# Kernel tuning notes

Measured on AMD Instinct MI355X. Metric: run time of the kernel, lower is better.

Reference implementation:

```python
import jax, jax.numpy as jnp
import numpy as np

THRESH = 0.9
NUM_HEADS = 4
HEAD_DIM = 8


def _ln(x, g, b, eps=1e-5):
    m = x.mean(-1, keepdims=True)
    v = ((x - m) ** 2).mean(-1, keepdims=True)
    return (x - m) * jax.lax.rsqrt(v + eps) * g + b


def setup_inputs() -> dict:
    key = jax.random.key(0)
    ks = jax.random.split(key, 32)
    n, d_in, h1, h2, d, ffn, nb = 4096, 512, 128, 64, 32, 64, 2

    def w(k, shape, fan_in):
        return jax.random.normal(k, shape, jnp.float32) * (1.0 / np.sqrt(fan_in))

    inp = {}
    inp["x"] = jax.random.normal(ks[0], (n, d_in), jnp.float32)
    # Autoencoder encoder: input_dim -> 128 -> 64 -> latent_dim
    inp["enc_w1"] = w(ks[1], (d_in, h1), d_in); inp["enc_b1"] = jnp.zeros((h1,), jnp.float32)
    inp["enc_w2"] = w(ks[2], (h1, h2), h1);     inp["enc_b2"] = jnp.zeros((h2,), jnp.float32)
    inp["enc_w3"] = w(ks[3], (h2, d), h2);      inp["enc_b3"] = jnp.zeros((d,), jnp.float32)
    # Transformer blocks (stacked over num_blocks=2)
    inp["wq"] = w(ks[4], (nb, d, d), d); inp["bq"] = jnp.zeros((nb, d), jnp.float32)
    inp["wk"] = w(ks[5], (nb, d, d), d); inp["bk"] = jnp.zeros((nb, d), jnp.float32)
    inp["wv"] = w(ks[6], (nb, d, d), d); inp["bv"] = jnp.zeros((nb, d), jnp.float32)
    inp["wo"] = w(ks[7], (nb, d, d), d); inp["bo"] = jnp.zeros((nb, d), jnp.float32)
    inp["ln1_g"] = jnp.ones((nb, d), jnp.float32);  inp["ln1_b"] = jnp.zeros((nb, d), jnp.float32)
    inp["ffn_w1"] = w(ks[8], (nb, d, ffn), d);      inp["ffn_b1"] = jnp.zeros((nb, ffn), jnp.float32)
    inp["ffn_w2"] = w(ks[9], (nb, ffn, d), ffn);    inp["ffn_b2"] = jnp.zeros((nb, d), jnp.float32)
    inp["ln2_g"] = jnp.ones((nb, d), jnp.float32);  inp["ln2_b"] = jnp.zeros((nb, d), jnp.float32)
    # Head: Linear(d,16) -> Tanh -> Linear(16, num_classes)
    inp["head_w1"] = w(ks[10], (d, 16), d);  inp["head_b1"] = jnp.zeros((16,), jnp.float32)
    inp["head_w2"] = w(ks[11], (16, 1), 16); inp["head_b2"] = jnp.zeros((1,), jnp.float32)
    return inp


def reference(x, enc_w1, enc_b1, enc_w2, enc_b2, enc_w3, enc_b3,
              wq, bq, wk, bk, wv, bv, wo, bo,
              ln1_g, ln1_b, ffn_w1, ffn_b1, ffn_w2, ffn_b2, ln2_g, ln2_b,
              head_w1, head_b1, head_w2, head_b2):
    # --- autoencoder encode: [n, d_in] -> [n, d] ---
    a = jax.nn.relu(x @ enc_w1 + enc_b1)
    a = jax.nn.relu(a @ enc_w2 + enc_b2)
    latent = a @ enc_w3 + enc_b3  # [n, d]

    # --- graph pool: cosine-sim threshold mask, per-node masked neighbor mean ---
    # self-similarity is 1.0 >= THRESH, so every node has >=1 neighbor (deg>=1)
    norms = jnp.linalg.norm(latent, axis=1, keepdims=True) + 1e-12
    normed = latent / norms
    sims = normed @ normed.T                                  # [n, n]
    mask = (sims >= THRESH).astype(latent.dtype)              # [n, n]
    deg = mask.sum(axis=1, keepdims=True)                     # [n, 1]
    pooled = latent + (mask @ latent) / deg                   # latent[i] + mean of neighbors

    # --- transformer blocks (post-LN, eval mode: dropout off) ---
    h = pooled[None]  # [1, n, d]
    n, d = pooled.shape
    nb = wq.shape[0]
    scale = 1.0 / np.sqrt(HEAD_DIM)
    for i in range(nb):
        q = (h @ wq[i] + bq[i]).reshape(1, n, NUM_HEADS, HEAD_DIM)
        k = (h @ wk[i] + bk[i]).reshape(1, n, NUM_HEADS, HEAD_DIM)
        v = (h @ wv[i] + bv[i]).reshape(1, n, NUM_HEADS, HEAD_DIM)
        scores = jnp.einsum('bqhd,bkhd->bhqk', q, k) * scale  # [1, H, n, n]
        attn = jax.nn.softmax(scores, axis=-1)
        o = jnp.einsum('bhqk,bkhd->bqhd', attn, v).reshape(1, n, d)
        o = o @ wo[i] + bo[i]
        h = _ln(h + o, ln1_g[i], ln1_b[i])
        f = jax.nn.relu(h @ ffn_w1[i] + ffn_b1[i]) @ ffn_w2[i] + ffn_b2[i]
        h = _ln(h + f, ln2_g[i], ln2_b[i])

    # --- head on mean-pooled sequence ---
    m = h.mean(axis=1)  # [1, d]
    out = jnp.tanh(m @ head_w1 + head_b1) @ head_w2 + head_b2  # [1, 1]
    return out.squeeze()
```

## Files before the change

kernel.cpp:

```cpp
#include <hip/hip_runtime.h>
#include <math.h>

#define N 4096
#define DIN 512
#define D 32
#define JC 8

__global__ __launch_bounds__(256) void enc_kernel(
    const float* __restrict__ x,
    const float* __restrict__ w1, const float* __restrict__ b1,
    const float* __restrict__ w2, const float* __restrict__ b2,
    const float* __restrict__ w3, const float* __restrict__ b3,
    float* __restrict__ latent, float* __restrict__ normed) {
  __shared__ float xs[8][512];
  __shared__ float h1p[4][8][128];
  __shared__ float h1s[8][128];
  __shared__ float h2s[8][64];
  __shared__ float w2s[128][64];
  __shared__ float w3s[64][32];
  const int t = threadIdx.x;
  const int r0 = blockIdx.x * 8;

  const float4* xg = (const float4*)(x + (size_t)r0 * DIN);
  float4* xl = (float4*)&xs[0][0];
#pragma unroll
  for (int i = 0; i < 4; ++i) xl[t + i * 256] = xg[t + i * 256];
  float4* w2l = (float4*)&w2s[0][0];
  const float4* w2g = (const float4*)w2;
#pragma unroll
  for (int i = 0; i < 8; ++i) w2l[t + i * 256] = w2g[t + i * 256];
  float4* w3l = (float4*)&w3s[0][0];
  const float4* w3g = (const float4*)w3;
#pragma unroll
  for (int i = 0; i < 2; ++i) w3l[t + i * 256] = w3g[t + i * 256];
  __syncthreads();

  {
    const int jc2 = (t & 63) * 2;
    const int kq = t >> 6;
    const int kb = kq * 128;
    float a0[8], a1[8];
#pragma unroll
    for (int r = 0; r < 8; ++r) { a0[r] = 0.f; a1[r] = 0.f; }
    const float* wp = w1 + (size_t)kb * 128 + jc2;

#define ENC_LD4(P0, P1, P2, P3, KK)                          \
    P0 = *(const float2*)&wp[(size_t)(KK) * 128];            \
    P1 = *(const float2*)&wp[(size_t)((KK) + 1) * 128];      \
    P2 = *(const float2*)&wp[(size_t)((KK) + 2) * 128];      \
    P3 = *(const float2*)&wp[(size_t)((KK) + 3) * 128];

#define ENC_STEP(W0, WA, WB, WC, KK)                                   \
    {                                                                  \
      _Pragma("unroll")                                                \
      for (int r = 0; r < 8; ++r) {                                    \
        const float4 xv = *(const float4*)&xs[r][kb + (KK)];           \
        a0[r] = fmaf(xv.x, W0.x, a0[r]); a1[r] = fmaf(xv.x, W0.y, a1[r]); \
        a0[r] = fmaf(xv.y, WA.x, a0[r]); a1[r] = fmaf(xv.y, WA.y, a1[r]); \
        a0[r] = fmaf(xv.z, WB.x, a0[r]); a1[r] = fmaf(xv.z, WB.y, a1[r]); \
        a0[r] = fmaf(xv.w, WC.x, a0[r]); a1[r] = fmaf(xv.w, WC.y, a1[r]); \
      }                                                                \
    }

    float2 A0, A1, A2, A3, B0, B1, B2, B3, C0, C1, C2, C3, D0, D1, D2, D3;
    ENC_LD4(A0, A1, A2, A3, 0)
    ENC_LD4(B0, B1, B2, B3, 4)
    ENC_LD4(C0, C1, C2, C3, 8)
    ENC_LD4(D0, D1, D2, D3, 12)
    for (int kk = 0; kk < 128; kk += 16) {
      ENC_STEP(A0, A1, A2, A3, kk + 0);
      if (kk + 16 < 128) { ENC_LD4(A0, A1, A2, A3, kk + 16) }
      ENC_STEP(B0, B1, B2, B3, kk + 4);
      if (kk + 20 < 128) { ENC_LD4(B0, B1, B2, B3, kk + 20) }
      ENC_STEP(C0, C1, C2, C3, kk + 8);
      if (kk + 24 < 128) { ENC_LD4(C0, C1, C2, C3, kk + 24) }
      ENC_STEP(D0, D1, D2, D3, kk + 12);
      if (kk + 28 < 128) { ENC_LD4(D0, D1, D2, D3, kk + 28) }
    }
#undef ENC_STEP
#undef ENC_LD4
#pragma unroll
    for (int r = 0; r < 8; ++r) {
      h1p[kq][r][jc2] = a0[r];
      h1p[kq][r][jc2 + 1] = a1[r];
    }
  }
  __syncthreads();

#pragma unroll
  for (int e0 = 0; e0 < 1024; e0 += 256) {
    const int e = e0 + t;
    const int r = e >> 7, c = e & 127;
    const float s = b1[c] + ((h1p[0][r][c] + h1p[1][r][c]) + (h1p[2][r][c] + h1p[3][r][c]));
    h1s[r][c] = fmaxf(s, 0.f);
  }
  __syncthreads();

  {
    const int j = t & 63, rg = t >> 6;
    const int ra = rg * 2, rb = ra + 1;
    float a0 = b2[j], a1 = b2[j];
#pragma unroll 8
    for (int kk = 0; kk < 128; ++kk) {
      const float w = w2s[kk][j];
      a0 = fmaf(h1s[ra][kk], w, a0);
      a1 = fmaf(h1s[rb][kk], w, a1);
    }
    h2s[ra][j] = fmaxf(a0, 0.f);
    h2s[rb][j] = fmaxf(a1, 0.f);
  }
  __syncthreads();

  {
    const int j = t & 31, og = t >> 5;
    float acc = b3[j];
#pragma unroll 8
    for (int kk = 0; kk < 64; ++kk) acc = fmaf(h2s[og][kk], w3s[kk][j], acc);
    float s2 = acc * acc;
    s2 += __shfl_xor(s2, 1);
    s2 += __shfl_xor(s2, 2);
    s2 += __shfl_xor(s2, 4);
    s2 += __shfl_xor(s2, 8);
    s2 += __shfl_xor(s2, 16);
    const float inv = 1.0f / (sqrtf(s2) + 1e-12f);
    const size_t off = (size_t)(r0 + og) * D + j;
    latent[off] = acc;
    normed[off] = acc * inv;
  }
}

__global__ __launch_bounds__(256) void pool_kernel(const float* __restrict__ normed,
                                                   const float* __restrict__ latent,
                                                   float* __restrict__ pacc,
                                                   float* __restrict__ pdeg) {
  __shared__ float smem[8192 + 256];
  float* nt = smem;
  float* lt = smem + 4096;
  float* degr = smem + 8192;
  const int t = threadIdx.x;
  const int il = t & 63, g = t >> 6;
  const int i0 = blockIdx.x * 64;
  const int j0 = blockIdx.y * 512;

  float ni[32];
  const float* nrow = normed + (size_t)(i0 + il) * D;
#pragma unroll
  for (int c = 0; c < 32; ++c) ni[c] = nrow[c];

  float acc[32];
#pragma unroll
  for (int c = 0; c < 32; ++c) acc[c] = 0.f;
  float deg = 0.f;

  for (int jt = j0; jt < j0 + 512; jt += 128) {
    __syncthreads();
    const float4* ng = (const float4*)(normed + (size_t)jt * D);
    const float4* lg = (const float4*)(latent + (size_t)jt * D);
    float4* ntl = (float4*)nt;
    float4* ltl = (float4*)lt;
#pragma unroll
    for (int i = 0; i < 4; ++i) {
      ntl[t + i * 256] = ng[t + i * 256];
      ltl[t + i * 256] = lg[t + i * 256];
    }
    __syncthreads();
    for (int jj = g; jj < 128; jj += 4) {
      const float* nr = nt + jj * 32;
      float s = 0.f;
#pragma unroll
      for (int c = 0; c < 32; ++c) s = fmaf(ni[c], nr[c], s);
      if (s >= 0.9f) {
        deg += 1.f;
        const float* lrow = lt + jj * 32;
#pragma unroll
        for (int c = 0; c < 32; ++c) acc[c] += lrow[c];
      }
    }
  }
  __syncthreads();
  float* accr = smem;
#pragma unroll
  for (int c = 0; c < 32; ++c) accr[(g * 64 + il) * 32 + c] = acc[c];
  degr[t] = deg;
  __syncthreads();
  for (int e = t; e < 64 * 32; e += 256) {
    const float s = accr[e] + accr[2048 + e] + accr[4096 + e] + accr[6144 + e];
    pacc[((size_t)blockIdx.y * N + i0 + (e >> 5)) * 32 + (e & 31)] = s;
  }
  if (t < 64) {
    pdeg[(size_t)blockIdx.y * N + i0 + t] = degr[t] + degr[64 + t] + degr[128 + t] + degr[192 + t];
  }
}

__global__ __launch_bounds__(256) void pool_combine(const float* __restrict__ latent,
                                                    const float* __restrict__ pacc,
                                                    const float* __restrict__ pdeg,
                                                    float* __restrict__ h) {
  const int e = blockIdx.x * 256 + threadIdx.x;
  const int i = e >> 5;
  float s = 0.f, dg = 0.f;
#pragma unroll
  for (int gch = 0; gch < JC; ++gch) {
    s += pacc[(size_t)gch * N * 32 + e];
    dg += pdeg[(size_t)gch * N + i];
  }
  h[e] = latent[e] + s / dg;
}

__global__ __launch_bounds__(256) void qkv_kernel(
    const float* __restrict__ h,
    const float* __restrict__ wq, const float* __restrict__ bq,
    const float* __restrict__ wk, const float* __restrict__ bk,
    const float* __restrict__ wv, const float* __restrict__ bv,
    float* __restrict__ q, float* __restrict__ k, float* __restrict__ v,
    int* __restrict__ kmax2i) {
  __shared__ float hs[32][32];
  __shared__ float wsm[3][32][32];
  __shared__ int kred[4];
  const int t = threadIdx.x;
  const int r0 = blockIdx.x * 32;
  if (t < 4) kred[t] = 0;
  ((float4*)&hs[0][0])[t] = ((const float4*)(h + (size_t)r0 * 32))[t];
  ((float4*)&wsm[0][0][0])[t] = ((const float4*)wq)[t];
  ((float4*)&wsm[1][0][0])[t] = ((const float4*)wk)[t];
  ((float4*)&wsm[2][0][0])[t] = ((const float4*)wv)[t];
  __syncthreads();
  const int j = t & 31, og = t >> 5;
  const int head = j >> 3;
  float aq[4], ak[4], av[4];
#pragma unroll
  for (int u = 0; u < 4; ++u) { aq[u] = bq[j]; ak[u] = bk[j]; av[u] = bv[j]; }
  for (int kk = 0; kk < 32; ++kk) {
    const float wqv = wsm[0][kk][j], wkv = wsm[1][kk][j], wvv = wsm[2][kk][j];
#pragma unroll
    for (int u = 0; u < 4; ++u) {
      const float hh = hs[og * 4 + u][kk];
      aq[u] = fmaf(hh, wqv, aq[u]);
      ak[u] = fmaf(hh, wkv, ak[u]);
      av[u] = fmaf(hh, wvv, av[u]);
    }
  }
  const float scale = 1.4426950408889634f * 0.35355339059327373f;
#pragma unroll
  for (int u = 0; u < 4; ++u) {
    const size_t off = (size_t)(r0 + og * 4 + u) * 32 + j;
    q[off] = aq[u] * scale;
    k[off] = ak[u];
    v[off] = av[u];
  }
#pragma unroll
  for (int u = 0; u < 4; ++u) {
    float s2 = ak[u] * ak[u];
    s2 += __shfl_xor(s2, 1);
    s2 += __shfl_xor(s2, 2);
    s2 += __shfl_xor(s2, 4);
    if ((j & 7) == 0) atomicMax(&kred[head], __float_as_int(s2));
  }
  __syncthreads();
  if (t < 4) atomicMax(&kmax2i[t], kred[t]);
}

__global__ __launch_bounds__(256) __attribute__((amdgpu_waves_per_eu(2, 2)))
void attn_kernel(const float* __restrict__ q,
                 const float* __restrict__ k,
                 const float* __restrict__ v,
                 const int* __restrict__ kmax2i,
                 float* __restrict__ apacc,
                 float* __restrict__ apl) {
  __shared__ float4 tiles[1024];
  float4* kls = tiles;
  float4* vls = tiles + 512;
  const int t = threadIdx.x;
  const int jg = t & 7, head = (t >> 3) & 3, rg = t >> 5;
  const int r0 = blockIdx.x * 64;
  const int j0 = blockIdx.y * (N / JC);

  const float km2 = __int_as_float(kmax2i[head]);

  float4 qa[8], qb[8], accA[8], accB[8];
  float mneg[8], l[8];
#pragma unroll
  for (int u = 0; u < 8; ++u) {
    const float* qr = q + (size_t)(r0 + rg * 8 + u) * 32 + head * 8;
    qa[u] = ((const float4*)qr)[0];
    qb[u] = ((const float4*)qr)[1];
    const float qn2 = qa[u].x * qa[u].x + qa[u].y * qa[u].y + qa[u].z * qa[u].z + qa[u].w * qa[u].w +
                      qb[u].x * qb[u].x + qb[u].y * qb[u].y + qb[u].z * qb[u].z + qb[u].w * qb[u].w;
    mneg[u] = -sqrtf(qn2 * km2);
    l[u] = 0.f;
    accA[u] = make_float4(0.f, 0.f, 0.f, 0.f);
    accB[u] = make_float4(0.f, 0.f, 0.f, 0.f);
  }

  float4 kr0, kr1, vr0, vr1;
  {
    const float4* kg = (const float4*)(k + (size_t)j0 * 32);
    const float4* vg = (const float4*)(v + (size_t)j0 * 32);
    kr0 = kg[t]; kr1 = kg[t + 256];
    vr0 = vg[t]; vr1 = vg[t + 256];
  }

  const int rA = t >> 3, slotA = (t & 7) ^ (rA & 7);
  const int g1 = t + 256;
  const int rB = g1 >> 3, slotB = (g1 & 7) ^ (rB & 7);

  const int h2 = head * 2;
  const int s0 = h2 ^ jg, s1 = (h2 + 1) ^ jg;
  for (int jt = j0; jt < j0 + (N / JC); jt += 64) {
    __syncthreads();
    kls[rA * 8 + slotA] = kr0;
    kls[rB * 8 + slotB] = kr1;
    vls[rA * 8 + slotA] = vr0;
    vls[rB * 8 + slotB] = vr1;
    __syncthreads();
    if (jt + 64 < j0 + (N / JC)) {
      const float4* kg = (const float4*)(k + (size_t)(jt + 64) * 32);
      const float4* vg = (const float4*)(v + (size_t)(jt + 64) * 32);
      kr0 = kg[t]; kr1 = kg[t + 256];
      vr0 = vg[t]; vr1 = vg[t + 256];
    }
#pragma unroll 2
    for (int it = 0; it < 8; ++it) {
      const int jj = it * 8 + jg;
      const float4 ka = kls[jj * 8 + s0];
      const float4 kb = kls[jj * 8 + s1];
      const float4 va = vls[jj * 8 + s0];
      const float4 vb = vls[jj * 8 + s1];
#pragma unroll
      for (int u = 0; u < 8; ++u) {
        float s = fmaf(qa[u].x, ka.x, mneg[u]);
        s = fmaf(qa[u].y, ka.y, s);
        s = fmaf(qa[u].z, ka.z, s);
        s = fmaf(qa[u].w, ka.w, s);
        s = fmaf(qb[u].x, kb.x, s);
        s = fmaf(qb[u].y, kb.y, s);
        s = fmaf(qb[u].z, kb.z, s);
        s = fmaf(qb[u].w, kb.w, s);
        const float p = __builtin_amdgcn_exp2f(s);
        l[u] += p;
        accA[u].x = fmaf(p, va.x, accA[u].x);
        accA[u].y = fmaf(p, va.y, accA[u].y);
        accA[u].z = fmaf(p, va.z, accA[u].z);
        accA[u].w = fmaf(p, va.w, accA[u].w);
        accB[u].x = fmaf(p, vb.x, accB[u].x);
        accB[u].y = fmaf(p, vb.y, accB[u].y);
        accB[u].z = fmaf(p, vb.z, accB[u].z);
        accB[u].w = fmaf(p, vb.w, accB[u].w);
      }
    }
  }
#pragma unroll
  for (int u = 0; u < 8; ++u) {
#pragma unroll
    for (int m = 1; m <= 4; m <<= 1) {
      accA[u].x += __shfl_xor(accA[u].x, m);
      accA[u].y += __shfl_xor(accA[u].y, m);
      accA[u].z += __shfl_xor(accA[u].z, m);
      accA[u].w += __shfl_xor(accA[u].w, m);
      accB[u].x += __shfl_xor(accB[u].x, m);
      accB[u].y += __shfl_xor(accB[u].y, m);
      accB[u].z += __shfl_xor(accB[u].z, m);
      accB[u].w += __shfl_xor(accB[u].w, m);
      l[u] += __shfl_xor(l[u], m);
    }
  }
  if (jg == 0) {
#pragma unroll
    for (int u = 0; u < 8; ++u) {
      const int row = r0 + rg * 8 + u;
      float* ap = apacc + (size_t)blockIdx.y * N * 32 + (size_t)row * 32 + head * 8;
      ((float4*)ap)[0] = accA[u];
      ((float4*)ap)[1] = accB[u];
      apl[(size_t)blockIdx.y * N * 4 + (size_t)row * 4 + head] = l[u];
    }
  }
}

__global__ __launch_bounds__(256) void acombine(const float* __restrict__ apacc,
                                                const float* __restrict__ apl,
                                                float* __restrict__ attno) {
  const int e = blockIdx.x * 256 + threadIdx.x;
  const int row = e >> 5;
  const int hh = (e >> 3) & 3;
  float L = 0.f, S = 0.f;
#pragma unroll
  for (int jc = 0; jc < JC; ++jc) {
    L += apl[(size_t)jc * N * 4 + row * 4 + hh];
    S += apacc[(size_t)jc * N * 32 + e];
  }
  attno[e] = S / L;
}

__global__ __launch_bounds__(256) void oln1_kernel(const float* __restrict__ attno,
                                                   const float* __restrict__ wo,
                                                   const float* __restrict__ bo,
                                                   const float* __restrict__ g,
                                                   const float* __restrict__ b,
                                                   float* __restrict__ h) {
  __shared__ float als[32][32];
  __shared__ float wols[32][32];
  __shared__ float ys[32][33];
  const int t = threadIdx.x;
  const int r0 = blockIdx.x * 32;
  ((float4*)&als[0][0])[t] = ((const float4*)(attno + (size_t)r0 * 32))[t];
  ((float4*)&wols[0][0])[t] = ((const float4*)wo)[t];
  __syncthreads();
  const int j = t & 31, og = t >> 5;
  float acc[4];
#pragma unroll
  for (int u = 0; u < 4; ++u) acc[u] = bo[j];
  for (int kk = 0; kk < 32; ++kk) {
    const float w = wols[kk][j];
#pragma unroll
    for (int u = 0; u < 4; ++u) acc[u] = fmaf(als[og * 4 + u][kk], w, acc[u]);
  }
#pragma unroll
  for (int u = 0; u < 4; ++u) {
    const int r = og * 4 + u;
    ys[r][j] = h[(size_t)(r0 + r) * 32 + j] + acc[u];
  }
  __syncthreads();
  if (t < 32) {
    float mu = 0.f;
#pragma unroll
    for (int c = 0; c < 32; ++c) mu += ys[t][c];
    mu *= (1.f / 32.f);
    float var = 0.f;
#pragma unroll
    for (int c = 0; c < 32; ++c) {
      const float dd = ys[t][c] - mu;
      var = fmaf(dd, dd, var);
    }
    var *= (1.f / 32.f);
    const float rs = rsqrtf(var + 1e-5f);
#pragma unroll
    for (int c = 0; c < 32; ++c)
      h[(size_t)(r0 + t) * 32 + c] = (ys[t][c] - mu) * rs * g[c] + b[c];
  }
}

__global__ __launch_bounds__(256) void ffn_kernel(const float* __restrict__ hin,
                                                  const float* __restrict__ w1,
                                                  const float* __restrict__ b1,
                                                  const float* __restrict__ w2,
                                                  const float* __restrict__ b2,
                                                  const float* __restrict__ g,
                                                  const float* __restrict__ bb,
                                                  float* __restrict__ h) {
  __shared__ float hs[32][32];
  __shared__ float w1s[32][64];
  __shared__ float w2s[64][32];
  __shared__ float mids[32][64];
  __shared__ float ys[32][33];
  const int t = threadIdx.x;
  const int r0 = blockIdx.x * 32;
  ((float4*)&hs[0][0])[t] = ((const float4*)(hin + (size_t)r0 * 32))[t];
#pragma unroll
  for (int i = 0; i < 2; ++i) {
    ((float4*)&w1s[0][0])[t + i * 256] = ((const float4*)w1)[t + i * 256];
    ((float4*)&w2s[0][0])[t + i * 256] = ((const float4*)w2)[t + i * 256];
  }
  __syncthreads();
  {
    const int jm = t & 63, gg = t >> 6;
    float acc[8];
#pragma unroll
    for (int u = 0; u < 8; ++u) acc[u] = b1[jm];
    for (int kk = 0; kk < 32; ++kk) {
      const float w = w1s[kk][jm];
#pragma unroll
      for (int u = 0; u < 8; ++u) acc[u] = fmaf(hs[gg * 8 + u][kk], w, acc[u]);
    }
#pragma unroll
    for (int u = 0; u < 8; ++u) mids[gg * 8 + u][jm] = fmaxf(acc[u], 0.f);
  }
  __syncthreads();
  {
    const int j = t & 31, og = t >> 5;
    float acc[4];
#pragma unroll
    for (int u = 0; u < 4; ++u) acc[u] = b2[j];
    for (int kk = 0; kk < 64; ++kk) {
      const float w = w2s[kk][j];
#pragma unroll
      for (int u = 0; u < 4; ++u) acc[u] = fmaf(mids[og * 4 + u][kk], w, acc[u]);
    }
#pragma unroll
    for (int u = 0; u < 4; ++u) {
      const int r = og * 4 + u;
      ys[r][j] = hs[r][j] + acc[u];
    }
  }
  __syncthreads();
  if (t < 32) {
    float mu = 0.f;
#pragma unroll
    for (int c = 0; c < 32; ++c) mu += ys[t][c];
    mu *= (1.f / 32.f);
    float var = 0.f;
#pragma unroll
    for (int c = 0; c < 32; ++c) {
      const float dd = ys[t][c] - mu;
      var = fmaf(dd, dd, var);
    }
    var *= (1.f / 32.f);
    const float rs = rsqrtf(var + 1e-5f);
#pragma unroll
    for (int c = 0; c < 32; ++c)
      h[(size_t)(r0 + t) * 32 + c] = (ys[t][c] - mu) * rs * g[c] + bb[c];
  }
}

__global__ __launch_bounds__(256) void headp_kernel(const float* __restrict__ h,
                                                    float* __restrict__ partial) {
  __shared__ float red[8][32];
  const int t = threadIdx.x;
  const int c = t & 31, rg = t >> 5;
  const int r0 = blockIdx.x * 64;
  float s = 0.f;
#pragma unroll
  for (int u = 0; u < 8; ++u) s += h[(size_t)(r0 + rg * 8 + u) * 32 + c];
  red[rg][c] = s;
  __syncthreads();
  if (t < 32) {
    float ss = 0.f;
#pragma unroll
    for (int u = 0; u < 8; ++u) ss += red[u][t];
    partial[blockIdx.x * 32 + t] = ss;
  }
}

__global__ __launch_bounds__(64) void headf_kernel(const float* __restrict__ partial,
                                                   const float* __restrict__ w1,
                                                   const float* __restrict__ b1,
                                                   const float* __restrict__ w2,
                                                   const float* __restrict__ b2,
                                                   float* __restrict__ out) {
  __shared__ float mls[32];
  __shared__ float tls[16];
  const int t = threadIdx.x;
  if (t < 32) {
    float s = 0.f;
    for (int bb = 0; bb < 64; ++bb) s += partial[bb * 32 + t];
    mls[t] = s * (1.f / 4096.f);
  }
  __syncthreads();
  if (t < 16) {
    float a = b1[t];
#pragma unroll
    for (int c = 0; c < 32; ++c) a = fmaf(mls[c], w1[c * 16 + t], a);
    tls[t] = tanhf(a);
  }
  __syncthreads();
  if (t == 0) {
    float o = b2[0];
#pragma unroll
    for (int jj = 0; jj < 16; ++jj) o = fmaf(tls[jj], w2[jj], o);
    out[0] = o;
  }
}

extern "C" void kernel_launch(void* const* d_in, const int* in_sizes, int n_in,
                              void* d_out, int out_size, void* d_ws, size_t ws_size,
                              hipStream_t stream) {
  const float* x      = (const float*)d_in[0];
  const float* enc_w1 = (const float*)d_in[1];
  const float* enc_b1 = (const float*)d_in[2];
  const float* enc_w2 = (const float*)d_in[3];
  const float* enc_b2 = (const float*)d_in[4];
  const float* enc_w3 = (const float*)d_in[5];
  const float* enc_b3 = (const float*)d_in[6];
  const float* wq     = (const float*)d_in[7];
  const float* bq     = (const float*)d_in[8];
  const float* wk     = (const float*)d_in[9];
  const float* bk     = (const float*)d_in[10];
  const float* wv     = (const float*)d_in[11];
  const float* bv     = (const float*)d_in[12];
  const float* wo     = (const float*)d_in[13];
  const float* bo     = (const float*)d_in[14];
  const float* ln1_g  = (const float*)d_in[15];
  const float* ln1_b  = (const float*)d_in[16];
  const float* ffn_w1 = (const float*)d_in[17];
  const float* ffn_b1 = (const float*)d_in[18];
  const float* ffn_w2 = (const float*)d_in[19];
  const float* ffn_b2 = (const float*)d_in[20];
  const float* ln2_g  = (const float*)d_in[21];
  const float* ln2_b  = (const float*)d_in[22];
  const float* head_w1 = (const float*)d_in[23];
  const float* head_b1 = (const float*)d_in[24];
  const float* head_w2 = (const float*)d_in[25];
  const float* head_b2 = (const float*)d_in[26];

  float* ws      = (float*)d_ws;
  float* latent  = ws;
  float* normed  = ws + 131072;
  float* h       = ws + 262144;
  float* q       = ws + 393216;
  float* k       = ws + 524288;
  float* v       = ws + 655360;
  float* attno   = ws + 786432;
  float* shreg   = ws + 917504;
  float* p_acc   = shreg;
  float* p_deg   = shreg + 1048576;
  float* a_acc   = shreg;
  float* a_l     = shreg + 1048576;
  int*   kmax2i  = (int*)(ws + 2097152);
  float* partial = ws + 2097216;

  hipMemsetAsync(kmax2i, 0, 8 * sizeof(int), stream);

  enc_kernel<<<512, 256, 0, stream>>>(x, enc_w1, enc_b1, enc_w2, enc_b2, enc_w3, enc_b3,
                                      latent, normed);
  pool_kernel<<<dim3(64, JC), 256, 0, stream>>>(normed, latent, p_acc, p_deg);
  pool_combine<<<512, 256, 0, stream>>>(latent, p_acc, p_deg, h);

  for (int blk = 0; blk < 2; ++blk) {
    qkv_kernel<<<128, 256, 0, stream>>>(h, wq + blk * 1024, bq + blk * 32,
                                        wk + blk * 1024, bk + blk * 32,
                                        wv + blk * 1024, bv + blk * 32, q, k, v,
                                        kmax2i + blk * 4);
    attn_kernel<<<dim3(64, JC), 256, 0, stream>>>(q, k, v, kmax2i + blk * 4, a_acc, a_l);
    acombine<<<512, 256, 0, stream>>>(a_acc, a_l, attno);
    oln1_kernel<<<128, 256, 0, stream>>>(attno, wo + blk * 1024, bo + blk * 32,
                                         ln1_g + blk * 32, ln1_b + blk * 32, h);
    ffn_kernel<<<128, 256, 0, stream>>>(h, ffn_w1 + blk * 2048, ffn_b1 + blk * 64,
                                        ffn_w2 + blk * 2048, ffn_b2 + blk * 32,
                                        ln2_g + blk * 32, ln2_b + blk * 32, h);
  }

  headp_kernel<<<64, 256, 0, stream>>>(h, partial);
  headf_kernel<<<1, 64, 0, stream>>>(partial, head_w1, head_b1, head_w2, head_b2, (float*)d_out);
}
```

Before: 180.6 us.

## Double-buffer K/V LDS tiles and prefetch next LDS row in attention loop

The attention kernel now keeps two LDS buffers for the K/V tiles. The next tile is written into the idle buffer after the current one has been computed, so each tile needs one barrier instead of two. Inside the inner loop, the next row's K/V float4 values are read from LDS one iteration ahead, in software-pipelined register form. This doubles LDS use to 32KB and raises register pressure, which could reduce occupancy or cause spills under the fixed waves_per_eu(2,2) setting.

```diff
diff --git a/kernel.cpp b/kernel.cpp
--- a/kernel.cpp
+++ b/kernel.cpp
@@ -267,9 +267,7 @@
                  const int* __restrict__ kmax2i,
                  float* __restrict__ apacc,
                  float* __restrict__ apl) {
-  __shared__ float4 tiles[1024];
-  float4* kls = tiles;
-  float4* vls = tiles + 512;
+  __shared__ float4 tiles[2048];
   const int t = threadIdx.x;
   const int jg = t & 7, head = (t >> 3) & 3, rg = t >> 5;
   const int r0 = blockIdx.x * 64;
@@ -292,6 +290,10 @@
     accB[u] = make_float4(0.f, 0.f, 0.f, 0.f);
   }
 
+  const int rA = t >> 3, slotA = (t & 7) ^ (rA & 7);
+  const int g1 = t + 256;
+  const int rB = g1 >> 3, slotB = (g1 & 7) ^ (rB & 7);
+
   float4 kr0, kr1, vr0, vr1;
   {
     const float4* kg = (const float4*)(k + (size_t)j0 * 32);
@@ -299,33 +301,38 @@
     kr0 = kg[t]; kr1 = kg[t + 256];
     vr0 = vg[t]; vr1 = vg[t + 256];
   }
-
-  const int rA = t >> 3, slotA = (t & 7) ^ (rA & 7);
-  const int g1 = t + 256;
-  const int rB = g1 >> 3, slotB = (g1 & 7) ^ (rB & 7);
+  tiles[rA * 8 + slotA] = kr0;
+  tiles[rB * 8 + slotB] = kr1;
+  tiles[512 + rA * 8 + slotA] = vr0;
+  tiles[512 + rB * 8 + slotB] = vr1;
+  __syncthreads();
 
   const int h2 = head * 2;
   const int s0 = h2 ^ jg, s1 = (h2 + 1) ^ jg;
-  for (int jt = j0; jt < j0 + (N / JC); jt += 64) {
-    __syncthreads();
-    kls[rA * 8 + slotA] = kr0;
-    kls[rB * 8 + slotB] = kr1;
-    vls[rA * 8 + slotA] = vr0;
-    vls[rB * 8 + slotB] = vr1;
-    __syncthreads();
-    if (jt + 64 < j0 + (N / JC)) {
-      const float4* kg = (const float4*)(k + (size_t)(jt + 64) * 32);
-      const float4* vg = (const float4*)(v + (size_t)(jt + 64) * 32);
+  int p = 0;
+  for (int tt = 0; tt < 8; ++tt) {
+    if (tt + 1 < 8) {
+      const float4* kg = (const float4*)(k + (size_t)(j0 + (tt + 1) * 64) * 32);
+      const float4* vg = (const float4*)(v + (size_t)(j0 + (tt + 1) * 64) * 32);
       kr0 = kg[t]; kr1 = kg[t + 256];
       vr0 = vg[t]; vr1 = vg[t + 256];
     }
+    const float4* kls = tiles + (p << 10);
+    const float4* vls = kls + 512;
+    float4 ka = kls[jg * 8 + s0];
+    float4 kb = kls[jg * 8 + s1];
+    float4 va = vls[jg * 8 + s0];
+    float4 vb = vls[jg * 8 + s1];
 #pragma unroll 2
     for (int it = 0; it < 8; ++it) {
-      const int jj = it * 8 + jg;
-      const float4 ka = kls[jj * 8 + s0];
-      const float4 kb = kls[jj * 8 + s1];
-      const float4 va = vls[jj * 8 + s0];
-      const float4 vb = vls[jj * 8 + s1];
+      float4 ka2, kb2, va2, vb2;
+      if (it < 7) {
+        const int jn = (it + 1) * 8 + jg;
+        ka2 = kls[jn * 8 + s0];
+        kb2 = kls[jn * 8 + s1];
+        va2 = vls[jn * 8 + s0];
+        vb2 = vls[jn * 8 + s1];
+      }
 #pragma unroll
       for (int u = 0; u < 8; ++u) {
         float s = fmaf(qa[u].x, ka.x, mneg[u]);
@@ -336,17 +343,28 @@
         s = fmaf(qb[u].y, kb.y, s);
         s = fmaf(qb[u].z, kb.z, s);
         s = fmaf(qb[u].w, kb.w, s);
-        const float p = __builtin_amdgcn_exp2f(s);
-        l[u] += p;
-        accA[u].x = fmaf(p, va.x, accA[u].x);
-        accA[u].y = fmaf(p, va.y, accA[u].y);
-        accA[u].z = fmaf(p, va.z, accA[u].z);
-        accA[u].w = fmaf(p, va.w, accA[u].w);
-        accB[u].x = fmaf(p, vb.x, accB[u].x);
-        accB[u].y = fmaf(p, vb.y, accB[u].y);
-        accB[u].z = fmaf(p, vb.z, accB[u].z);
-        accB[u].w = fmaf(p, vb.w, accB[u].w);
+        const float p2 = __builtin_amdgcn_exp2f(s);
+        l[u] += p2;
+        accA[u].x = fmaf(p2, va.x, accA[u].x);
+        accA[u].y = fmaf(p2, va.y, accA[u].y);
+        accA[u].z = fmaf(p2, va.z, accA[u].z);
+        accA[u].w = fmaf(p2, va.w, accA[u].w);
+        accB[u].x = fmaf(p2, vb.x, accB[u].x);
+        accB[u].y = fmaf(p2, vb.y, accB[u].y);
+        accB[u].z = fmaf(p2, vb.z, accB[u].z);
+        accB[u].w = fmaf(p2, vb.w, accB[u].w);
       }
+      if (it < 7) { ka = ka2; kb = kb2; va = va2; vb = vb2; }
+    }
+    if (tt + 1 < 8) {
+      float4* klsn = tiles + ((p ^ 1) << 10);
+      float4* vlsn = klsn + 512;
+      klsn[rA * 8 + slotA] = kr0;
+      klsn[rB * 8 + slotB] = kr1;
+      vlsn[rA * 8 + slotA] = vr0;
+      vlsn[rB * 8 + slotB] = vr1;
+      __syncthreads();
+      p ^= 1;
     }
   }
 #pragma unroll
```

Measured after the change: 188.9 us. 1.05x slower.
